# Performance work log

Measured on AMD Instinct MI355X. Metric: run time of the kernel, lower is better.

The kernel has to match this reference:

```python
import jax, jax.numpy as jnp
import numpy as np

B, T, D, H = 512, 128, 384, 6
DH = D // H  # 64
DFF = 4 * D  # 1536
EPS = 1e-5


def layer_norm(x, g, b):
    mu = jnp.mean(x, axis=-1, keepdims=True)
    var = jnp.var(x, axis=-1, keepdims=True)
    return (x - mu) * jax.lax.rsqrt(var + EPS) * g + b


def setup_inputs() -> dict:
    key = jax.random.key(0)
    ks = jax.random.split(key, 12)
    s = lambda *sh: 1.0 / np.sqrt(sh[0])
    return {
        "x": jax.random.normal(ks[0], (B, T, D), dtype=jnp.float32),
        "Wq": jax.random.normal(ks[1], (D, D), dtype=jnp.float32) * s(D),
        "Wk": jax.random.normal(ks[2], (D, D), dtype=jnp.float32) * s(D),
        "Wv": jax.random.normal(ks[3], (D, D), dtype=jnp.float32) * s(D),
        "Wo": jax.random.normal(ks[4], (D, D), dtype=jnp.float32) * s(D),
        "bo": jnp.zeros((D,), jnp.float32),
        "W1": jax.random.normal(ks[5], (D, DFF), dtype=jnp.float32) * s(D),
        "b1": jnp.zeros((DFF,), jnp.float32),
        "W2": jax.random.normal(ks[6], (DFF, D), dtype=jnp.float32) * s(DFF),
        "b2": jnp.zeros((D,), jnp.float32),
        "g1": jnp.ones((D,), jnp.float32),
        "be1": jnp.zeros((D,), jnp.float32),
        "g2": jnp.ones((D,), jnp.float32),
        "be2": jnp.zeros((D,), jnp.float32),
    }


def reference(x, Wq, Wk, Wv, Wo, bo, W1, b1, W2, b2, g1, be1, g2, be2):
    # --- multi-head causal self-attention on layer_norm1(x) ---
    h = layer_norm(x, g1, be1)
    q = (h @ Wq).reshape(B, T, H, DH)
    k = (h @ Wk).reshape(B, T, H, DH)
    v = (h @ Wv).reshape(B, T, H, DH)
    scores = jnp.einsum("bthd,bshd->bhts", q, k) * (DH ** -0.5)  # [B,H,T,T]
    causal = jnp.tril(jnp.ones((T, T), dtype=bool))
    scores = jnp.where(causal, scores, -jnp.inf)
    attn = jax.nn.softmax(scores, axis=-1)
    o = jnp.einsum("bhts,bshd->bthd", attn, v).reshape(B, T, D)
    x = x + o @ Wo + bo
    # --- feed-forward on layer_norm2(x) ---
    h2 = layer_norm(x, g2, be2)
    ff = jax.nn.relu(h2 @ W1 + b1) @ W2 + b2
    return x + ff
```

## Files before the change

kernel.cpp:

```cpp
#include <hip/hip_runtime.h>

#define B_   512
#define T_   128
#define D_   384
#define H_   6
#define DH_  64
#define DFF_ 1536
#define NROW (B_*T_)

typedef __attribute__((ext_vector_type(8))) short bf16x8;
typedef __attribute__((ext_vector_type(4))) float f32x4;

__device__ __forceinline__ unsigned short f2bf(float f) {
  union { float f; unsigned u; } v; v.f = f;
  unsigned r = v.u + 0x7fffu + ((v.u >> 16) & 1u);
  return (unsigned short)(r >> 16);
}

#define GLDS16(gp, lp)                                                     \
  __builtin_amdgcn_global_load_lds(                                        \
      (const __attribute__((address_space(1))) void*)(gp),                 \
      (__attribute__((address_space(3))) void*)(lp), 16, 0, 0)

#define BAR_LGKM() asm volatile("s_waitcnt lgkmcnt(0)\n\ts_barrier" ::: "memory")

__global__ void wt_kernel(const float* __restrict__ W, unsigned short* __restrict__ WT,
                          int K, int Nn) {
  int id = blockIdx.x * 256 + threadIdx.x;
  if (id >= K * Nn) return;
  int n = id % Nn, kk = id / Nn;
  WT[(size_t)n * K + kk] = f2bf(W[(size_t)kk * Nn + n]);
}

__global__ void pack_w1(const unsigned short* __restrict__ W1T,
                        unsigned short* __restrict__ W1P) {
  int tid = blockIdx.x * 256 + threadIdx.x;
  int lane = tid & 63, frag = tid >> 6;
  int k = frag % 12, t2 = frag / 12;
  int mi = t2 & 1, t3 = t2 >> 1;
  int w = t3 & 3, c = t3 >> 2;
  int l15 = lane & 15, lq = lane >> 4;
  int r = c * 128 + w * 32 + mi * 16 + l15;
  int col = k * 32 + lq * 8;
  *(int4*)(W1P + (size_t)tid * 8) = *(const int4*)(W1T + (size_t)r * 384 + col);
}
__global__ void pack_w2(const unsigned short* __restrict__ W2T,
                        unsigned short* __restrict__ W2P) {
  int tid = blockIdx.x * 256 + threadIdx.x;
  int lane = tid & 63, frag = tid >> 6;
  int kk = frag & 3, t2 = frag >> 2;
  int c = t2 % 12, t3 = t2 / 12;
  int mi = t3 % 6, w = t3 / 6;
  int l15 = lane & 15, lq = lane >> 4;
  int r = w * 96 + mi * 16 + l15;
  int col = c * 128 + kk * 32 + lq * 8;
  *(int4*)(W2P + (size_t)tid * 8) = *(const int4*)(W2T + (size_t)r * 1536 + col);
}

__global__ __launch_bounds__(256) void ln_kernel(const float* __restrict__ x,
                                                 const float* __restrict__ g,
                                                 const float* __restrict__ be,
                                                 unsigned short* __restrict__ out) {
  int row = (blockIdx.x * 256 + threadIdx.x) >> 6;
  int l = threadIdx.x & 63;
  const float* xr = x + (size_t)row * D_;
  float v[6]; float s = 0.f, ss = 0.f;
  #pragma unroll
  for (int i = 0; i < 6; ++i) { v[i] = xr[l + i*64]; s += v[i]; ss += v[i]*v[i]; }
  #pragma unroll
  for (int m = 1; m < 64; m <<= 1) { s += __shfl_xor(s, m); ss += __shfl_xor(ss, m); }
  float mu  = s * (1.f / D_);
  float var = ss * (1.f / D_) - mu * mu;
  float rs  = rsqrtf(var + 1e-5f);
  unsigned short* orow = out + (size_t)row * D_;
  #pragma unroll
  for (int i = 0; i < 6; ++i) {
    int c = l + i*64;
    orow[c] = f2bf((v[i] - mu) * rs * g[c] + be[c]);
  }
}

__global__ __launch_bounds__(512, 4) void qkv_gemm(
    const unsigned short* __restrict__ h, const unsigned short* __restrict__ wP,
    unsigned short* __restrict__ qkv)
{
  __shared__ __align__(16) char smem[25600];
  int tid = threadIdx.x, w = tid >> 6, l = tid & 63;
  int l15 = l & 15, lq = l >> 4;
  size_t R0 = (size_t)blockIdx.x * 32;

  {
    int row = tid >> 4, gi = row >> 4, l15w = row & 15;
    const unsigned short* src = h + (R0 + row) * 384 + (tid & 15) * 24;
    #pragma unroll
    for (int i = 0; i < 3; ++i) {
      int col = (tid & 15) * 24 + i * 8;
      int k = col >> 5, lqw = (col >> 3) & 3;
      *(int4*)(smem + (gi*12 + k)*1024 + (lqw*16 + l15w)*16) = *(const int4*)(src + i*8);
    }
  }
  __syncthreads();

  f32x4 acc[9][2];
  #pragma unroll
  for (int c = 0; c < 9; ++c)
    #pragma unroll
    for (int ni = 0; ni < 2; ++ni) acc[c][ni] = (f32x4){0.f, 0.f, 0.f, 0.f};

  const unsigned short* wb = wP + l * 8;

  #define LDG(dst, cb, k)                                                    \
    { _Pragma("unroll") for (int ci = 0; ci < 3; ++ci)                       \
        dst[ci] = *(const bf16x8*)(wb + (((cb)+ci)*8 + w) * 6144 + (k) * 512); }

  #define CMPG(buf, cb)                                                      \
    { _Pragma("unroll") for (int ci = 0; ci < 3; ++ci)                       \
        _Pragma("unroll") for (int ni = 0; ni < 2; ++ni)                     \
          acc[(cb)+ci][ni] = __builtin_amdgcn_mfma_f32_16x16x32_bf16(        \
              buf[ci], bfr[ni], acc[(cb)+ci][ni], 0, 0, 0); }

  bf16x8 a0[3], a1[3], a2[3];
  LDG(a0, 0, 0)

  for (int k = 0; k < 12; ++k) {
    bf16x8 bfr[2];
    #pragma unroll
    for (int ni = 0; ni < 2; ++ni)
      bfr[ni] = *(const bf16x8*)(smem + (ni*12 + k)*1024 + l*16);
    int kn = (k < 11) ? k + 1 : 11;
    LDG(a1, 3, k)
    __builtin_amdgcn_s_setprio(1); CMPG(a0, 0) __builtin_amdgcn_s_setprio(0);
    LDG(a2, 6, k)
    __builtin_amdgcn_s_setprio(1); CMPG(a1, 3) __builtin_amdgcn_s_setprio(0);
    LDG(a0, 0, kn)
    __builtin_amdgcn_s_setprio(1); CMPG(a2, 6) __builtin_amdgcn_s_setprio(0);
  }
  #undef LDG
  #undef CMPG

  __syncthreads();
  #pragma unroll
  for (int buf = 0; buf < 3; ++buf) {
    #pragma unroll
    for (int ci = 0; ci < 3; ++ci) {
      int c = buf * 3 + ci;
      #pragma unroll
      for (int ni = 0; ni < 2; ++ni) {
        int row = ni * 16 + l15;
        ushort4 pk;
        pk.x = f2bf(acc[c][ni][0]);
        pk.y = f2bf(acc[c][ni][1]);
        pk.z = f2bf(acc[c][ni][2]);
        pk.w = f2bf(acc[c][ni][3]);
        *(ushort4*)(smem + row * 784 + ci * 256 + w * 32 + lq * 8) = pk;
      }
    }
    __syncthreads();
    {
      int row = tid >> 4;
      unsigned short* obase = qkv + (size_t)buf * NROW * 384 + (R0 + row) * 384;
      #pragma unroll
      for (int i = 0; i < 3; ++i) {
        int ob = (tid & 15) * 16 + i * 256;
        *(int4*)(obase + (ob >> 1)) = *(const int4*)(smem + row * 784 + ob);
      }
    }
    __syncthreads();
  }
}

template<int EPI>
__global__ __launch_bounds__(256) void gemm_bt(const unsigned short* __restrict__ A,
                                               const unsigned short* __restrict__ BT,
                                               void* __restrict__ Cc,
                                               const float* __restrict__ bias,
                                               const float* __restrict__ res,
                                               int Nn, int K) {
  __shared__ unsigned short As[2][128][32];
  __shared__ unsigned short Bs[2][128][32];
  int tid = threadIdx.x, w = tid >> 6, l = tid & 63;
  int wr = w >> 1, wc = w & 1;

  int ncol = gridDim.y;
  int nwg  = gridDim.x * ncol;
  int lin  = blockIdx.y * gridDim.x + blockIdx.x;
  int cpx  = nwg >> 3;
  int swz  = (lin & 7) * cpx + (lin >> 3);
  size_t R0 = (size_t)(swz / ncol) * 128;
  int C0 = (swz % ncol) * 128;

  int seg0 = (w * 2 + 0) * 16;
  int seg1 = (w * 2 + 1) * 16;
  int srow0 = seg0 + (l >> 2);
  int srow1 = seg1 + (l >> 2);
  int scol  = (l & 3) * 8;

  const unsigned short* ga0 = A  + (R0 + srow0) * K + scol;
  const unsigned short* ga1 = A  + (R0 + srow1) * K + scol;
  const unsigned short* gb0 = BT + (size_t)(C0 + srow0) * K + scol;
  const unsigned short* gb1 = BT + (size_t)(C0 + srow1) * K + scol;

  f32x4 acc[4][4];
  #pragma unroll
  for (int i = 0; i < 4; ++i)
    #pragma unroll
    for (int j = 0; j < 4; ++j) acc[i][j] = (f32x4){0.f, 0.f, 0.f, 0.f};

  GLDS16(ga0, &As[0][seg0][0]);
  GLDS16(ga1, &As[0][seg1][0]);
  GLDS16(gb0, &Bs[0][seg0][0]);
  GLDS16(gb1, &Bs[0][seg1][0]);
  ga0 += 32; ga1 += 32; gb0 += 32; gb1 += 32;

  int nk = K >> 5;
  for (int t = 0; t < nk; ++t) {
    int cur = t & 1;
    __syncthreads();
    if (t + 1 < nk) {
      GLDS16(ga0, &As[cur ^ 1][seg0][0]);
      GLDS16(ga1, &As[cur ^ 1][seg1][0]);
      GLDS16(gb0, &Bs[cur ^ 1][seg0][0]);
      GLDS16(gb1, &Bs[cur ^ 1][seg1][0]);
      ga0 += 32; ga1 += 32; gb0 += 32; gb1 += 32;
    }
    bf16x8 af[4], bf[4];
    #pragma unroll
    for (int mi = 0; mi < 4; ++mi)
      af[mi] = *(const bf16x8*)(&As[cur][wr*64 + mi*16 + (l & 15)][(l >> 4) * 8]);
    #pragma unroll
    for (int ni = 0; ni < 4; ++ni)
      bf[ni] = *(const bf16x8*)(&Bs[cur][wc*64 + ni*16 + (l & 15)][(l >> 4) * 8]);
    #pragma unroll
    for (int mi = 0; mi < 4; ++mi)
      #pragma unroll
      for (int ni = 0; ni < 4; ++ni)
        acc[mi][ni] = __builtin_amdgcn_mfma_f32_16x16x32_bf16(af[mi], bf[ni], acc[mi][ni], 0, 0, 0);
  }

  #pragma unroll
  for (int mi = 0; mi < 4; ++mi) {
    #pragma unroll
    for (int ni = 0; ni < 4; ++ni) {
      int col = C0 + wc*64 + ni*16 + (l & 15);
      #pragma unroll
      for (int j = 0; j < 4; ++j) {
        size_t row = R0 + wr*64 + mi*16 + ((l >> 4) << 2) + j;
        float vv = acc[mi][ni][j];
        ((float*)Cc)[row * Nn + col] = vv + bias[col] + res[row * Nn + col];
      }
    }
  }
}

#define LDA3(dst, pA, k0)                                                    \
  { _Pragma("unroll") for (int kq = 0; kq < 3; ++kq)                         \
      dst[kq] = *(const bf16x8*)((pA) + ((k0) + kq) * 512); }

#define CMP3(buf, k0, acc)                                                   \
  { _Pragma("unroll") for (int kq = 0; kq < 3; ++kq) {                       \
      bf16x8 bfr[4];                                                         \
      _Pragma("unroll") for (int ni = 0; ni < 4; ++ni)                       \
        bfr[ni] = *(const bf16x8*)(smem + (ni*12 + (k0)+kq)*1024 + l*16);    \
      _Pragma("unroll") for (int ni = 0; ni < 4; ++ni)                       \
        acc[ni] = __builtin_amdgcn_mfma_f32_16x16x32_bf16(                   \
            buf[kq], bfr[ni], acc[ni], 0, 0, 0);                             \
    } }

__global__ __launch_bounds__(512, 4) void ffn_fused(
    const unsigned short* __restrict__ h2,
    const unsigned short* __restrict__ w1P,
    const unsigned short* __restrict__ w2P,
    const float* __restrict__ b1,
    const float* __restrict__ b2,
    float* __restrict__ out)
{
  extern __shared__ __align__(16) char smem[];
  int tid = threadIdx.x, w = tid >> 6, l = tid & 63;
  int l15 = l & 15, lq = l >> 4;
  size_t R0 = (size_t)blockIdx.x * 64;

  {
    int row = tid >> 3, gi = row >> 4, l15w = row & 15;
    int cbase = (tid & 7) * 48;
    const unsigned short* src = h2 + (R0 + row) * 384 + cbase;
    #pragma unroll
    for (int i = 0; i < 6; ++i) {
      int col = cbase + i * 8;
      int k = col >> 5, lqw = (col >> 3) & 3;
      *(int4*)(smem + (gi*12 + k)*1024 + (lqw*16 + l15w)*16) = *(const int4*)(src + i*8);
    }
  }
  __syncthreads();

  f32x4 oacc[3][4];
  #pragma unroll
  for (int i = 0; i < 3; ++i)
    #pragma unroll
    for (int j = 0; j < 4; ++j) oacc[i][j] = (f32x4){0.f, 0.f, 0.f, 0.f};

  const unsigned short* w1b = w1P + w * 6144  + l * 8;
  const unsigned short* w2b = w2P + w * 73728 + l * 8;

  #define LDV(dst, pV, kk)                                                   \
    { _Pragma("unroll") for (int mi = 0; mi < 3; ++mi)                       \
        dst[mi] = *(const bf16x8*)((pV) + mi * 24576 + (kk) * 512); }

  #define CMPV(buf, kk, pb)                                                  \
    { bf16x8 bv[4];                                                          \
      _Pragma("unroll") for (int ni = 0; ni < 4; ++ni)                       \
        bv[ni] = *(const bf16x8*)(smem + (pb) + (ni*4 + (kk))*1024 + l*16);  \
      _Pragma("unroll") for (int mi = 0; mi < 3; ++mi)                       \
        _Pragma("unroll") for (int ni = 0; ni < 4; ++ni)                     \
          oacc[mi][ni] = __builtin_amdgcn_mfma_f32_16x16x32_bf16(            \
              buf[mi], bv[ni], oacc[mi][ni], 0, 0, 0);                       \
    }

  bf16x8 afA[3], afB[3];
  bf16x8 avA[3], avB[3];

  LDA3(afA, w1b, 0)

  for (int c = 0; c < 12; ++c) {
    const unsigned short* pA = w1b + (size_t)c * 49152;
    const unsigned short* pV = w2b + c * 2048;
    unsigned pb = 49152u + (unsigned)(c & 1) * 16384u;

    f32x4 pacc[4];
    #pragma unroll
    for (int j = 0; j < 4; ++j) pacc[j] = (f32x4){0.f, 0.f, 0.f, 0.f};

    LDA3(afB, pA, 3)
    __builtin_amdgcn_s_setprio(1); CMP3(afA, 0, pacc) __builtin_amdgcn_s_setprio(0);
    LDA3(afA, pA, 6)
    __builtin_amdgcn_s_setprio(1); CMP3(afB, 3, pacc) __builtin_amdgcn_s_setprio(0);
    LDA3(afB, pA, 9)
    __builtin_amdgcn_s_setprio(1); CMP3(afA, 6, pacc) __builtin_amdgcn_s_setprio(0);
    LDV(avA, pV, 0)
    __builtin_amdgcn_s_setprio(1); CMP3(afB, 9, pacc) __builtin_amdgcn_s_setprio(0);

    {
      int fcb = c * 128 + w * 16 + lq * 4;
      float4 bb = *(const float4*)(b1 + fcb);
      unsigned pw = pb + (unsigned)((w >> 1) * 1024 +
                    (((w & 1) * 2 + (lq >> 1)) * 16 + l15) * 16 + (lq & 1) * 8);
      #pragma unroll
      for (int ni = 0; ni < 4; ++ni) {
        float p0 = pacc[ni][0] + bb.x;
        float p1 = pacc[ni][1] + bb.y;
        float p2 = pacc[ni][2] + bb.z;
        float p3 = pacc[ni][3] + bb.w;
        ushort4 pk;
        pk.x = f2bf(p0 > 0.f ? p0 : 0.f);
        pk.y = f2bf(p1 > 0.f ? p1 : 0.f);
        pk.z = f2bf(p2 > 0.f ? p2 : 0.f);
        pk.w = f2bf(p3 > 0.f ? p3 : 0.f);
        *(ushort4*)(smem + pw + ni * 4096) = pk;
      }
    }
    BAR_LGKM();

    const unsigned short* pAn = w1b + (size_t)(c < 11 ? c + 1 : 11) * 49152;
    LDV(avB, pV, 1)
    __builtin_amdgcn_s_setprio(1); CMPV(avA, 0, pb) __builtin_amdgcn_s_setprio(0);
    LDV(avA, pV, 2)
    __builtin_amdgcn_s_setprio(1); CMPV(avB, 1, pb) __builtin_amdgcn_s_setprio(0);
    LDV(avB, pV, 3)
    __builtin_amdgcn_s_setprio(1); CMPV(avA, 2, pb) __builtin_amdgcn_s_setprio(0);
    LDA3(afA, pAn, 0)
    __builtin_amdgcn_s_setprio(1); CMPV(avB, 3, pb) __builtin_amdgcn_s_setprio(0);
  }
  #undef LDV
  #undef CMPV

  #pragma unroll
  for (int mi = 0; mi < 3; ++mi) {
    int ocb = w * 48 + mi * 16 + lq * 4;
    float4 b2v = *(const float4*)(b2 + ocb);
    #pragma unroll
    for (int ni = 0; ni < 4; ++ni) {
      size_t row = R0 + ni * 16 + l15;
      float* op = out + row * D_ + ocb;
      float4 r = *(const float4*)op;
      float4 o;
      o.x = oacc[mi][ni][0] + b2v.x + r.x;
      o.y = oacc[mi][ni][1] + b2v.y + r.y;
      o.z = oacc[mi][ni][2] + b2v.z + r.z;
      o.w = oacc[mi][ni][3] + b2v.w + r.w;
      *(float4*)op = o;
    }
  }
}

__global__ __launch_bounds__(256) void attn_kernel(const unsigned short* __restrict__ q,
                                                   const unsigned short* __restrict__ k,
                                                   const unsigned short* __restrict__ v,
                                                   unsigned short* __restrict__ o) {
  __shared__ __align__(16) char smem[52224];
  unsigned short (*Ks)[72]       = (unsigned short(*)[72])smem;
  unsigned short (*Ps)[32][136]  = (unsigned short(*)[32][136])smem;
  unsigned short (*Vt)[136]      = (unsigned short(*)[136])(smem + 34816);

  int bh = blockIdx.x;
  int b = bh / H_, h = bh % H_;
  int tid = threadIdx.x, w = tid >> 6, l = tid & 63;

  const unsigned short* kb = k + ((size_t)b * T_) * D_ + h * DH_;
  const unsigned short* vb = v + ((size_t)b * T_) * D_ + h * DH_;
  #pragma unroll
  for (int it = 0; it < 4; ++it) {
    int id = it * 256 + tid;
    int s = id >> 3, c8 = (id & 7) * 8;
    int4 kv = *(const int4*)(kb + (size_t)s * D_ + c8);
    *(int4*)(&Ks[s][c8]) = kv;
    int4 vv = *(const int4*)(vb + (size_t)s * D_ + c8);
    const unsigned short* pe = (const unsigned short*)&vv;
    #pragma unroll
    for (int j2 = 0; j2 < 8; ++j2) Vt[c8 + j2][s] = pe[j2];
  }
  __syncthreads();

  const unsigned short* qbp = q + ((size_t)b * T_) * D_ + h * DH_;
  int rowbase = w * 32;
  bf16x8 aq[2][2];
  #pragma unroll
  for (int mi = 0; mi < 2; ++mi)
    #pragma unroll
    for (int ks = 0; ks < 2; ++ks)
      aq[mi][ks] = *(const bf16x8*)(qbp + (size_t)(rowbase + mi*16 + (l & 15)) * D_
                                        + ks*32 + ((l >> 4) << 3));

  f32x4 accs[2][8];
  #pragma unroll
  for (int i = 0; i < 2; ++i)
    #pragma unroll
    for (int j = 0; j < 8; ++j) accs[i][j] = (f32x4){0.f, 0.f, 0.f, 0.f};
  #pragma unroll
  for (int ks = 0; ks < 2; ++ks) {
    bf16x8 bk[8];
    #pragma unroll
    for (int ni = 0; ni < 8; ++ni)
      bk[ni] = *(const bf16x8*)(&Ks[ni*16 + (l & 15)][ks*32 + ((l >> 4) << 3)]);
    __builtin_amdgcn_s_setprio(1);
    #pragma unroll
    for (int mi = 0; mi < 2; ++mi)
      #pragma unroll
      for (int ni = 0; ni < 8; ++ni)
        accs[mi][ni] = __builtin_amdgcn_mfma_f32_16x16x32_bf16(aq[mi][ks], bk[ni], accs[mi][ni], 0, 0, 0);
    __builtin_amdgcn_s_setprio(0);
  }
  __syncthreads();

  #pragma unroll
  for (int mi = 0; mi < 2; ++mi) {
    #pragma unroll
    for (int j = 0; j < 4; ++j) {
      int t = rowbase + mi*16 + ((l >> 4) << 2) + j;
      float mx = -1e30f;
      #pragma unroll
      for (int ni = 0; ni < 8; ++ni) {
        int scol = ni*16 + (l & 15);
        float sv = accs[mi][ni][j] * 0.125f;
        sv = (scol <= t) ? sv : -1e30f;
        accs[mi][ni][j] = sv;
        mx = fmaxf(mx, sv);
      }
      mx = fmaxf(mx, __shfl_xor(mx, 1));
      mx = fmaxf(mx, __shfl_xor(mx, 2));
      mx = fmaxf(mx, __shfl_xor(mx, 4));
      mx = fmaxf(mx, __shfl_xor(mx, 8));
      float sum = 0.f;
      #pragma unroll
      for (int ni = 0; ni < 8; ++ni) {
        float e = __expf(accs[mi][ni][j] - mx);
        accs[mi][ni][j] = e;
        sum += e;
      }
      sum += __shfl_xor(sum, 1);
      sum += __shfl_xor(sum, 2);
      sum += __shfl_xor(sum, 4);
      sum += __shfl_xor(sum, 8);
      float inv = 1.f / sum;
      #pragma unroll
      for (int ni = 0; ni < 8; ++ni)
        Ps[w][mi*16 + ((l >> 4) << 2) + j][ni*16 + (l & 15)] = f2bf(accs[mi][ni][j] * inv);
    }
  }
  __syncthreads();

  f32x4 acco[2][4];
  #pragma unroll
  for (int i = 0; i < 2; ++i)
    #pragma unroll
    for (int j = 0; j < 4; ++j) acco[i][j] = (f32x4){0.f, 0.f, 0.f, 0.f};
  #pragma unroll
  for (int ks = 0; ks < 4; ++ks) {
    bf16x8 ap[2], bv[4];
    #pragma unroll
    for (int mi = 0; mi < 2; ++mi)
      ap[mi] = *(const bf16x8*)(&Ps[w][mi*16 + (l & 15)][ks*32 + ((l >> 4) << 3)]);
    #pragma unroll
    for (int ni = 0; ni < 4; ++ni)
      bv[ni] = *(const bf16x8*)(&Vt[ni*16 + (l & 15)][ks*32 + ((l >> 4) << 3)]);
    __builtin_amdgcn_s_setprio(1);
    #pragma unroll
    for (int mi = 0; mi < 2; ++mi)
      #pragma unroll
      for (int ni = 0; ni < 4; ++ni)
        acco[mi][ni] = __builtin_amdgcn_mfma_f32_16x16x32_bf16(ap[mi], bv[ni], acco[mi][ni], 0, 0, 0);
    __builtin_amdgcn_s_setprio(0);
  }

  unsigned short* ob = o + ((size_t)b * T_) * D_ + h * DH_;
  #pragma unroll
  for (int mi = 0; mi < 2; ++mi)
    #pragma unroll
    for (int ni = 0; ni < 4; ++ni)
      #pragma unroll
      for (int j = 0; j < 4; ++j) {
        int t = rowbase + mi*16 + ((l >> 4) << 2) + j;
        int d = ni*16 + (l & 15);
        ob[(size_t)t * D_ + d] = f2bf(acco[mi][ni][j]);
      }
}

extern "C" void kernel_launch(void* const* d_in, const int* in_sizes, int n_in,
                              void* d_out, int out_size, void* d_ws, size_t ws_size,
                              hipStream_t stream) {
  const float* x   = (const float*)d_in[0];
  const float* Wq  = (const float*)d_in[1];
  const float* Wk  = (const float*)d_in[2];
  const float* Wv  = (const float*)d_in[3];
  const float* Wo  = (const float*)d_in[4];
  const float* bo  = (const float*)d_in[5];
  const float* W1  = (const float*)d_in[6];
  const float* b1  = (const float*)d_in[7];
  const float* W2  = (const float*)d_in[8];
  const float* b2  = (const float*)d_in[9];
  const float* g1  = (const float*)d_in[10];
  const float* be1 = (const float*)d_in[11];
  const float* g2  = (const float*)d_in[12];
  const float* be2 = (const float*)d_in[13];

  char* ws = (char*)d_ws;
  unsigned short* hb    = (unsigned short*)(ws);
  unsigned short* qb    = (unsigned short*)(ws +  50331648);
  unsigned short* kbuf  = (unsigned short*)(ws + 100663296);
  unsigned short* vbuf  = (unsigned short*)(ws + 150994944);
  unsigned short* wqT   = (unsigned short*)(ws + 201326592);
  unsigned short* woT   = wqT + 442368;
  unsigned short* w1T   = woT + 147456;
  unsigned short* w2T   = w1T + 589824;
  unsigned short* w1P   = w2T + 589824;
  unsigned short* w2P   = w1P + 589824;
  unsigned short* wqkvP = w2P + 589824;
  float* x2 = (float*)d_out;
  (void)kbuf; (void)vbuf;

  hipFuncSetAttribute(reinterpret_cast<const void*>(ffn_fused),
                      hipFuncAttributeMaxDynamicSharedMemorySize, 81920);

  wt_kernel<<<dim3(576),  256, 0, stream>>>(Wq, wqT,          384, 384);
  wt_kernel<<<dim3(576),  256, 0, stream>>>(Wk, wqT + 147456, 384, 384);
  wt_kernel<<<dim3(576),  256, 0, stream>>>(Wv, wqT + 294912, 384, 384);
  wt_kernel<<<dim3(576),  256, 0, stream>>>(Wo, woT,          384, 384);
  wt_kernel<<<dim3(2304), 256, 0, stream>>>(W1, w1T, 384, 1536);
  wt_kernel<<<dim3(2304), 256, 0, stream>>>(W2, w2T, 1536, 384);
  pack_w1<<<dim3(216), 256, 0, stream>>>(wqT, wqkvP);
  pack_w1<<<dim3(288), 256, 0, stream>>>(w1T, w1P);
  pack_w2<<<dim3(288), 256, 0, stream>>>(w2T, w2P);

  ln_kernel<<<dim3(NROW / 4), 256, 0, stream>>>(x, g1, be1, hb);

  qkv_gemm<<<dim3(NROW / 32), 512, 0, stream>>>(hb, wqkvP, qb);

  attn_kernel<<<dim3(B_ * H_), 256, 0, stream>>>(qb, kbuf, vbuf, qb);

  gemm_bt<1><<<dim3(NROW / 128, 3), 256, 0, stream>>>(qb, woT, x2, bo, x, 384, 384);

  ln_kernel<<<dim3(NROW / 4), 256, 0, stream>>>((const float*)x2, g2, be2, hb);

  ffn_fused<<<dim3(NROW / 64), 512, 81920, stream>>>(hb, w1P, w2P, b1, b2, x2);
}
```

Baseline: 438.8 us.

## Fuse output projection, residual add and second LayerNorm into one kernel

Replaces the tiled Wo GEMM and the separate LayerNorm kernel with one kernel. Each block owns 32 full rows, multiplies them by a pre-packed Wo streamed from global into registers, adds bias and residual, then computes LayerNorm in shared memory and writes both x2 (fp32) and h2 (bf16). This drops the x2 re-read and one launch. The cost is weight reloads per small row tile and a different loop structure that must match the pack_w1 layout.

```diff
diff --git a/kernel.cpp b/kernel.cpp
--- a/kernel.cpp
+++ b/kernel.cpp
@@ -16,11 +16,6 @@
   unsigned r = v.u + 0x7fffu + ((v.u >> 16) & 1u);
   return (unsigned short)(r >> 16);
 }
-
-#define GLDS16(gp, lp)                                                     \
-  __builtin_amdgcn_global_load_lds(                                        \
-      (const __attribute__((address_space(1))) void*)(gp),                 \
-      (__attribute__((address_space(3))) void*)(lp), 16, 0, 0)
 
 #define BAR_LGKM() asm volatile("s_waitcnt lgkmcnt(0)\n\ts_barrier" ::: "memory")
 
@@ -169,85 +164,118 @@
   }
 }
 
-template<int EPI>
-__global__ __launch_bounds__(256) void gemm_bt(const unsigned short* __restrict__ A,
-                                               const unsigned short* __restrict__ BT,
-                                               void* __restrict__ Cc,
-                                               const float* __restrict__ bias,
-                                               const float* __restrict__ res,
-                                               int Nn, int K) {
-  __shared__ unsigned short As[2][128][32];
-  __shared__ unsigned short Bs[2][128][32];
+__global__ __launch_bounds__(512, 4) void wo_ln(
+    const unsigned short* __restrict__ o,
+    const unsigned short* __restrict__ wP,
+    const float* __restrict__ bo, const float* __restrict__ xres,
+    const float* __restrict__ g, const float* __restrict__ be,
+    float* __restrict__ x2out,
+    unsigned short* __restrict__ h2out)
+{
+  __shared__ __align__(16) char smem[50176];
   int tid = threadIdx.x, w = tid >> 6, l = tid & 63;
-  int wr = w >> 1, wc = w & 1;
-
-  int ncol = gridDim.y;
-  int nwg  = gridDim.x * ncol;
-  int lin  = blockIdx.y * gridDim.x + blockIdx.x;
-  int cpx  = nwg >> 3;
-  int swz  = (lin & 7) * cpx + (lin >> 3);
-  size_t R0 = (size_t)(swz / ncol) * 128;
-  int C0 = (swz % ncol) * 128;
-
-  int seg0 = (w * 2 + 0) * 16;
-  int seg1 = (w * 2 + 1) * 16;
-  int srow0 = seg0 + (l >> 2);
-  int srow1 = seg1 + (l >> 2);
-  int scol  = (l & 3) * 8;
-
-  const unsigned short* ga0 = A  + (R0 + srow0) * K + scol;
-  const unsigned short* ga1 = A  + (R0 + srow1) * K + scol;
-  const unsigned short* gb0 = BT + (size_t)(C0 + srow0) * K + scol;
-  const unsigned short* gb1 = BT + (size_t)(C0 + srow1) * K + scol;
-
-  f32x4 acc[4][4];
-  #pragma unroll
-  for (int i = 0; i < 4; ++i)
-    #pragma unroll
-    for (int j = 0; j < 4; ++j) acc[i][j] = (f32x4){0.f, 0.f, 0.f, 0.f};
-
-  GLDS16(ga0, &As[0][seg0][0]);
-  GLDS16(ga1, &As[0][seg1][0]);
-  GLDS16(gb0, &Bs[0][seg0][0]);
-  GLDS16(gb1, &Bs[0][seg1][0]);
-  ga0 += 32; ga1 += 32; gb0 += 32; gb1 += 32;
-
-  int nk = K >> 5;
-  for (int t = 0; t < nk; ++t) {
-    int cur = t & 1;
-    __syncthreads();
-    if (t + 1 < nk) {
-      GLDS16(ga0, &As[cur ^ 1][seg0][0]);
-      GLDS16(ga1, &As[cur ^ 1][seg1][0]);
-      GLDS16(gb0, &Bs[cur ^ 1][seg0][0]);
-      GLDS16(gb1, &Bs[cur ^ 1][seg1][0]);
-      ga0 += 32; ga1 += 32; gb0 += 32; gb1 += 32;
-    }
-    bf16x8 af[4], bf[4];
-    #pragma unroll
-    for (int mi = 0; mi < 4; ++mi)
-      af[mi] = *(const bf16x8*)(&As[cur][wr*64 + mi*16 + (l & 15)][(l >> 4) * 8]);
-    #pragma unroll
-    for (int ni = 0; ni < 4; ++ni)
-      bf[ni] = *(const bf16x8*)(&Bs[cur][wc*64 + ni*16 + (l & 15)][(l >> 4) * 8]);
-    #pragma unroll
-    for (int mi = 0; mi < 4; ++mi)
-      #pragma unroll
-      for (int ni = 0; ni < 4; ++ni)
-        acc[mi][ni] = __builtin_amdgcn_mfma_f32_16x16x32_bf16(af[mi], bf[ni], acc[mi][ni], 0, 0, 0);
-  }
-
-  #pragma unroll
-  for (int mi = 0; mi < 4; ++mi) {
-    #pragma unroll
-    for (int ni = 0; ni < 4; ++ni) {
-      int col = C0 + wc*64 + ni*16 + (l & 15);
-      #pragma unroll
-      for (int j = 0; j < 4; ++j) {
-        size_t row = R0 + wr*64 + mi*16 + ((l >> 4) << 2) + j;
-        float vv = acc[mi][ni][j];
-        ((float*)Cc)[row * Nn + col] = vv + bias[col] + res[row * Nn + col];
-      }
+  int l15 = l & 15, lq = l >> 4;
+  size_t R0 = (size_t)blockIdx.x * 32;
+
+  {
+    int row = tid >> 4, gi = row >> 4, l15w = row & 15;
+    const unsigned short* src = o + (R0 + row) * 384 + (tid & 15) * 24;
+    #pragma unroll
+    for (int i = 0; i < 3; ++i) {
+      int col = (tid & 15) * 24 + i * 8;
+      int k = col >> 5, lqw = (col >> 3) & 3;
+      *(int4*)(smem + (gi*12 + k)*1024 + (lqw*16 + l15w)*16) = *(const int4*)(src + i*8);
+    }
+  }
+  __syncthreads();
+
+  f32x4 acc[3][2];
+  #pragma unroll
+  for (int c = 0; c < 3; ++c)
+    #pragma unroll
+    for (int ni = 0; ni < 2; ++ni) acc[c][ni] = (f32x4){0.f, 0.f, 0.f, 0.f};
+
+  const unsigned short* wb = wP + l * 8;
+
+  #define LDGW(dst, k)                                                       \
+    { _Pragma("unroll") for (int ci = 0; ci < 3; ++ci)                       \
+        dst[ci] = *(const bf16x8*)(wb + (ci*8 + w) * 6144 + (k) * 512); }
+
+  #define CMPW(buf)                                                          \
+    { _Pragma("unroll") for (int ci = 0; ci < 3; ++ci)                       \
+        _Pragma("unroll") for (int ni = 0; ni < 2; ++ni)                     \
+          acc[ci][ni] = __builtin_amdgcn_mfma_f32_16x16x32_bf16(             \
+              buf[ci], bfr[ni], acc[ci][ni], 0, 0, 0); }
+
+  bf16x8 aA[3], aB[3];
+  LDGW(aA, 0)
+  for (int k = 0; k < 12; k += 2) {
+    bf16x8 bfr[2];
+    #pragma unroll
+    for (int ni = 0; ni < 2; ++ni)
+      bfr[ni] = *(const bf16x8*)(smem + (ni*12 + k)*1024 + l*16);
+    LDGW(aB, k + 1)
+    __builtin_amdgcn_s_setprio(1); CMPW(aA) __builtin_amdgcn_s_setprio(0);
+    #pragma unroll
+    for (int ni = 0; ni < 2; ++ni)
+      bfr[ni] = *(const bf16x8*)(smem + (ni*12 + k + 1)*1024 + l*16);
+    int kn = (k + 2 < 12) ? k + 2 : 11;
+    LDGW(aA, kn)
+    __builtin_amdgcn_s_setprio(1); CMPW(aB) __builtin_amdgcn_s_setprio(0);
+  }
+  #undef LDGW
+  #undef CMPW
+
+  __syncthreads();
+  #pragma unroll
+  for (int ci = 0; ci < 3; ++ci) {
+    int col = ci * 128 + w * 16 + lq * 4;
+    float4 bb = *(const float4*)(bo + col);
+    #pragma unroll
+    for (int ni = 0; ni < 2; ++ni) {
+      int row = ni * 16 + l15;
+      float4 r = *(const float4*)(xres + (R0 + row) * 384 + col);
+      float4 v;
+      v.x = acc[ci][ni][0] + bb.x + r.x;
+      v.y = acc[ci][ni][1] + bb.y + r.y;
+      v.z = acc[ci][ni][2] + bb.z + r.z;
+      v.w = acc[ci][ni][3] + bb.w + r.w;
+      *(float4*)(smem + row * 1568 + col * 4) = v;
+    }
+  }
+  __syncthreads();
+
+  {
+    int row = tid >> 4, t16 = tid & 15;
+    const char* rbase = smem + row * 1568;
+    float4 vv[6];
+    float s = 0.f, ss = 0.f;
+    #pragma unroll
+    for (int i = 0; i < 6; ++i) {
+      vv[i] = *(const float4*)(rbase + (t16 + i * 16) * 16);
+      s  += vv[i].x + vv[i].y + vv[i].z + vv[i].w;
+      ss += vv[i].x*vv[i].x + vv[i].y*vv[i].y + vv[i].z*vv[i].z + vv[i].w*vv[i].w;
+    }
+    s += __shfl_xor(s, 1); ss += __shfl_xor(ss, 1);
+    s += __shfl_xor(s, 2); ss += __shfl_xor(ss, 2);
+    s += __shfl_xor(s, 4); ss += __shfl_xor(ss, 4);
+    s += __shfl_xor(s, 8); ss += __shfl_xor(ss, 8);
+    float mu = s * (1.f / 384.f);
+    float rs = rsqrtf(ss * (1.f / 384.f) - mu * mu + 1e-5f);
+    float* xrow = x2out + (R0 + row) * 384;
+    unsigned short* hrow = h2out + (R0 + row) * 384;
+    #pragma unroll
+    for (int i = 0; i < 6; ++i) {
+      int c4 = t16 + i * 16;
+      float4 ga = *(const float4*)(g  + c4 * 4);
+      float4 ba = *(const float4*)(be + c4 * 4);
+      *(float4*)(xrow + c4 * 4) = vv[i];
+      ushort4 pk;
+      pk.x = f2bf((vv[i].x - mu) * rs * ga.x + ba.x);
+      pk.y = f2bf((vv[i].y - mu) * rs * ga.y + ba.y);
+      pk.z = f2bf((vv[i].z - mu) * rs * ga.z + ba.z);
+      pk.w = f2bf((vv[i].w - mu) * rs * ga.w + ba.w);
+      *(ushort4*)(hrow + c4 * 4) = pk;
     }
   }
 }
@@ -553,6 +581,7 @@
   unsigned short* w1P   = w2T + 589824;
   unsigned short* w2P   = w1P + 589824;
   unsigned short* wqkvP = w2P + 589824;
+  unsigned short* woP   = wqkvP + 442368;
   float* x2 = (float*)d_out;
   (void)kbuf; (void)vbuf;
 
@@ -566,6 +595,7 @@
   wt_kernel<<<dim3(2304), 256, 0, stream>>>(W1, w1T, 384, 1536);
   wt_kernel<<<dim3(2304), 256, 0, stream>>>(W2, w2T, 1536, 384);
   pack_w1<<<dim3(216), 256, 0, stream>>>(wqT, wqkvP);
+  pack_w1<<<dim3(72),  256, 0, stream>>>(woT, woP);
   pack_w1<<<dim3(288), 256, 0, stream>>>(w1T, w1P);
   pack_w2<<<dim3(288), 256, 0, stream>>>(w2T, w2P);
 
@@ -575,9 +605,7 @@
 
   attn_kernel<<<dim3(B_ * H_), 256, 0, stream>>>(qb, kbuf, vbuf, qb);
 
-  gemm_bt<1><<<dim3(NROW / 128, 3), 256, 0, stream>>>(qb, woT, x2, bo, x, 384, 384);
-
-  ln_kernel<<<dim3(NROW / 4), 256, 0, stream>>>((const float*)x2, g2, be2, hb);
+  wo_ln<<<dim3(NROW / 32), 512, 0, stream>>>(qb, woP, bo, x, g2, be2, x2, hb);
 
   ffn_fused<<<dim3(NROW / 64), 512, 81920, stream>>>(hb, w1P, w2P, b1, b2, x2);
 }
```

Result: faster. 422.3 us (-3.8%).
